# Performance work log

Measured on AMD Instinct MI355X. Metric: run time of the kernel, lower is better.

The kernel has to match this reference:

```python
import jax, jax.numpy as jnp
import numpy as np

B, N, NS, C, H = 2, 2048, 2048, 512, 8
HD = C // H
SCALE = HD ** -0.5
NEG = -10000.0


def setup_inputs() -> dict:
    key = jax.random.key(0)
    ks = jax.random.split(key, 9)
    q = jax.random.normal(ks[0], (B, N, C), dtype=jnp.float32)
    k = jax.random.normal(ks[1], (B, NS, C), dtype=jnp.float32)
    v = jax.random.normal(ks[2], (B, NS, C), dtype=jnp.float32)
    # 1.0 marks invalid support positions (gets -10000 added)
    supp_valid_mask = (jax.random.uniform(ks[3], (B, NS)) < 0.2).astype(jnp.float32)
    # binary fg/bg support mask used for cycle consistency
    supp_mask = jax.random.randint(ks[4], (B, NS), 0, 2, dtype=jnp.int32)
    w = 0.02
    Wq = jax.random.normal(ks[5], (C, C), dtype=jnp.float32) * w
    Wk = jax.random.normal(ks[6], (C, C), dtype=jnp.float32) * w
    Wv = jax.random.normal(ks[7], (C, C), dtype=jnp.float32) * w
    Wproj = jax.random.normal(ks[8], (C, C), dtype=jnp.float32) * w
    return {"q": q, "k": k, "v": v, "supp_valid_mask": supp_valid_mask,
            "supp_mask": supp_mask, "Wq": Wq, "Wk": Wk, "Wv": Wv, "Wproj": Wproj}


def reference(q, k, v, supp_valid_mask, supp_mask, Wq, Wk, Wv, Wproj):
    b, n, c = q.shape
    ns = k.shape[1]
    # linear projections (torch Linear: x @ W^T), split heads -> [B,H,N,HD]
    qh = (q @ Wq.T).reshape(b, n, H, HD).transpose(0, 2, 1, 3)
    kh = (k @ Wk.T).reshape(b, ns, H, HD).transpose(0, 2, 1, 3)
    vh = (v @ Wv.T).reshape(b, ns, H, HD).transpose(0, 2, 1, 3)
    attn = jnp.einsum('bhnd,bhmd->bhnm', qh, kh) * SCALE  # [B,H,N,NS]

    # cycle-consistency association (vectorized over heads)
    k2q = jnp.argmax(attn, axis=2)                    # [B,H,NS] idx into N
    q2k = jnp.argmax(attn, axis=3)                    # [B,H,N]  idx into NS
    re_map_idx = jnp.take_along_axis(q2k, k2q, axis=2)  # [B,H,NS]
    sm = jnp.broadcast_to(supp_mask[:, None, :], (b, H, ns))
    re_map_mask = jnp.take_along_axis(sm, re_map_idx, axis=2)
    asso = sm == re_map_mask                          # [B,H,NS] bool

    # mark cycle-inconsistent positions invalid (eval: ass_drop is identity)
    valid = jnp.broadcast_to(supp_valid_mask[:, None, :], (b, H, ns))
    valid = jnp.where(asso, valid, 1.0)

    attn = attn + (valid * NEG)[:, :, None, :]
    attn = jax.nn.softmax(attn, axis=-1)
    x = jnp.einsum('bhnm,bhmd->bhnd', attn, vh)       # [B,H,N,HD]
    x = x.transpose(0, 2, 1, 3).reshape(b, n, c)
    return x @ Wproj.T
```

## Files before the change

kernel.cpp:

```cpp
#include <hip/hip_runtime.h>
#include <hip/hip_bf16.h>
#include <stdint.h>

#define H_ 8
#define NS_ 2048
#define C_ 512
#define HD_ 64
#define SCALE_ 0.125f
#define NEG_ -10000.0f
#define LOG2E_ 1.4426950408889634f
#define MFIX_ 4.0f

typedef _Float16 f16x8_t __attribute__((ext_vector_type(8)));
typedef _Float16 f16x4_t __attribute__((ext_vector_type(4)));
typedef __fp16 h16x2_t __attribute__((ext_vector_type(2)));
typedef float f32x4_t __attribute__((ext_vector_type(4)));

#define MFMAH(a, b, c) __builtin_amdgcn_mfma_f32_16x16x32_f16(a, b, c, 0, 0, 0)

__device__ inline f16x8_t load_h8(const _Float16* p) {
    return *reinterpret_cast<const f16x8_t*>(p);
}

__device__ inline void gload_lds16(const void* g, void* l) {
    __builtin_amdgcn_global_load_lds(
        (const __attribute__((address_space(1))) unsigned int*)g,
        (__attribute__((address_space(3))) unsigned int*)l, 16, 0, 0);
}

__device__ inline unsigned orderF(float v) {
    unsigned u = __float_as_uint(v);
    return (u & 0x80000000u) ? ~u : (u | 0x80000000u);
}
__device__ inline unsigned long long packVR(float v, int idx) {
    return ((unsigned long long)orderF(v) << 32) | (unsigned)(~idx);
}
__device__ inline unsigned long long max64(unsigned long long a, unsigned long long b) {
    return a > b ? a : b;
}
__device__ inline unsigned long long shflx64(unsigned long long x, int m) {
    unsigned lo = (unsigned)x, hi = (unsigned)(x >> 32);
    lo = __shfl_xor(lo, m, 64);
    hi = __shfl_xor(hi, m, 64);
    return ((unsigned long long)hi << 32) | lo;
}

__global__ __launch_bounds__(256) void wsplit4(
        const float* __restrict__ w0, const float* __restrict__ w1,
        const float* __restrict__ w2, const float* __restrict__ w3,
        _Float16* __restrict__ hi, _Float16* __restrict__ lo)
{
    const int i = blockIdx.x * 256 + threadIdx.x;
    const int y = blockIdx.y;
    const float* src = (y == 0) ? w0 : (y == 1) ? w1 : (y == 2) ? w2 : w3;
    const float4 v = reinterpret_cast<const float4*>(src)[i];
    f16x4_t hv, lv;
    hv[0] = (_Float16)v.x; hv[1] = (_Float16)v.y;
    hv[2] = (_Float16)v.z; hv[3] = (_Float16)v.w;
    lv[0] = (_Float16)(v.x - (float)hv[0]);
    lv[1] = (_Float16)(v.y - (float)hv[1]);
    lv[2] = (_Float16)(v.z - (float)hv[2]);
    lv[3] = (_Float16)(v.w - (float)hv[3]);
    const size_t o = ((size_t)y << 16) + i;
    reinterpret_cast<f16x4_t*>(hi)[o] = hv;
    reinterpret_cast<f16x4_t*>(lo)[o] = lv;
}

__global__ __launch_bounds__(256) void proj_gemm(
        const float* __restrict__ qin, const float* __restrict__ kin,
        const float* __restrict__ vin,
        const _Float16* __restrict__ wHall, const _Float16* __restrict__ wLall,
        _Float16* __restrict__ qhi, _Float16* __restrict__ qlo,
        _Float16* __restrict__ khi, _Float16* __restrict__ klo,
        _Float16* __restrict__ vT)
{
    __shared__ __attribute__((aligned(16))) _Float16 Wsh[2][2][4096];
    const int zz = blockIdx.z;
    const float* A32 = (zz == 0) ? qin : (zz == 1) ? kin : vin;
    const _Float16* Wh = wHall + ((size_t)zz << 18);
    const _Float16* Wl = wLall + ((size_t)zz << 18);
    const int t = threadIdx.x, w = t >> 6, lane = t & 63;
    const int m16 = lane & 15, quad = lane >> 4;
    const int bm = blockIdx.x << 7, bn = blockIdx.y << 6;
    const int r0 = bm + (w << 5) + m16, r1 = r0 + 16;
    const int krow = lane >> 3, kblk = (lane & 7) ^ (krow & 7);
    const int e = m16 & 7;
    const int s00 = (quad ^ e) << 3, s01 = ((4 + quad) ^ e) << 3;
    const f32x4_t z = {0.f, 0.f, 0.f, 0.f};
    f32x4_t acc[2][4];
    #pragma unroll
    for (int rs = 0; rs < 2; rs++)
        #pragma unroll
        for (int tl = 0; tl < 4; tl++) acc[rs][tl] = z;

    auto stageW = [&](int buf, int kc) {
        #pragma unroll
        for (int ci = 0; ci < 4; ci++) {
            const int pp = (w << 2) + ci;
            const int s = pp >> 3, pj = pp & 7;
            const _Float16* src = (s ? Wl : Wh)
                + (size_t)(bn + (pj << 3) + krow) * C_ + kc + (kblk << 3);
            gload_lds16(src, &Wsh[buf][s][pj << 9]);
        }
    };
    auto loadA = [&](int kc, f16x8_t* d) {
        #pragma unroll
        for (int rs = 0; rs < 2; rs++) {
            const float* pr = A32 + (size_t)(rs ? r1 : r0) * C_ + kc + (quad << 3);
            #pragma unroll
            for (int seg = 0; seg < 2; seg++) {
                f16x8_t hv, lv;
                #pragma unroll
                for (int i = 0; i < 8; i++) {
                    const float x = pr[seg * 32 + i];
                    const _Float16 hh = (_Float16)x;
                    hv[i] = hh;
                    lv[i] = (_Float16)(x - (float)hh);
                }
                d[rs * 4 + seg] = hv;
                d[rs * 4 + seg + 2] = lv;
            }
        }
    };

    f16x8_t cA[8], nA[8];
    stageW(0, 0);
    loadA(0, cA);
    for (int ch = 0; ch < 8; ch++) {
        __syncthreads();
        if (ch + 1 < 8) {
            stageW((ch + 1) & 1, (ch + 1) << 6);
            loadA((ch + 1) << 6, nA);
        }
        const _Float16* W0 = Wsh[ch & 1][0];
        const _Float16* W1 = Wsh[ch & 1][1];
        #pragma unroll
        for (int tl = 0; tl < 4; tl++) {
            const int j64 = ((tl << 4) + m16) << 6;
            const f16x8_t bh0 = load_h8(&W0[j64 + s00]);
            const f16x8_t bh1 = load_h8(&W0[j64 + s01]);
            const f16x8_t bl0 = load_h8(&W1[j64 + s00]);
            const f16x8_t bl1 = load_h8(&W1[j64 + s01]);
            f32x4_t c0 = acc[0][tl];
            c0 = MFMAH(cA[0], bh0, c0); c0 = MFMAH(cA[1], bh1, c0);
            c0 = MFMAH(cA[2], bh0, c0); c0 = MFMAH(cA[3], bh1, c0);
            c0 = MFMAH(cA[0], bl0, c0); c0 = MFMAH(cA[1], bl1, c0);
            acc[0][tl] = c0;
            f32x4_t c1 = acc[1][tl];
            c1 = MFMAH(cA[4], bh0, c1); c1 = MFMAH(cA[5], bh1, c1);
            c1 = MFMAH(cA[6], bh0, c1); c1 = MFMAH(cA[7], bh1, c1);
            c1 = MFMAH(cA[4], bl0, c1); c1 = MFMAH(cA[5], bl1, c1);
            acc[1][tl] = c1;
        }
        #pragma unroll
        for (int i = 0; i < 8; i++) cA[i] = nA[i];
    }
    const int by = blockIdx.y;
    _Float16* o1 = (zz == 0) ? qhi : khi;
    _Float16* o2 = (zz == 0) ? qlo : klo;
    #pragma unroll
    for (int rs = 0; rs < 2; rs++) {
        #pragma unroll
        for (int tl = 0; tl < 4; tl++) {
            #pragma unroll
            for (int r = 0; r < 4; r++) {
                const int gr = bm + (w << 5) + (rs << 4) + (quad << 2) + r;
                const float val = acc[rs][tl][r];
                const int b = gr >> 11, n = gr & 2047;
                const int d = (tl << 4) + m16;
                const int bh = (b << 3) + by;
                if (zz == 2) {
                    const int kp = (((n >> 2) & 3) << 3) | (((n >> 4) & 1) << 2) | (n & 3);
                    vT[(((size_t)((bh << 6) + (n >> 5)) << 6) + d) * 32 + kp] = (_Float16)val;
                } else {
                    const size_t idx = ((((size_t)bh << 11) + n) << 6) + d;
                    const _Float16 hh = (_Float16)val;
                    o1[idx] = hh;
                    o2[idx] = (_Float16)(val - (float)hh);
                }
            }
        }
    }
}

__global__ __launch_bounds__(256) void argmax_mfma(
        const _Float16* __restrict__ qhi, const _Float16* __restrict__ qlo,
        const _Float16* __restrict__ khi, const _Float16* __restrict__ klo,
        unsigned long long* __restrict__ rowP, unsigned long long* __restrict__ colP)
{
    __shared__ __attribute__((aligned(16))) _Float16 Ksh[2][4096];
    __shared__ unsigned long long colbest[512];
    const int bx = blockIdx.x;
    const int bh = ((bx & 7) << 1) | (bx >> 9);
    const int mid = (bx >> 3) & 63;
    const int rt = mid & 15;
    const int ks = mid >> 4;
    const int t = threadIdx.x, w = t >> 6, lane = t & 63;
    const int m16 = lane & 15, quad = lane >> 4;
    const int wrow = (rt << 7) + (w << 5);
    const size_t qoff0 = ((((size_t)bh << 11) + wrow + m16) << 6) + (quad << 3);
    const size_t qoff1 = qoff0 + 1024;
    const f16x8_t a00h = load_h8(qhi + qoff0), a01h = load_h8(qhi + qoff0 + 32);
    const f16x8_t a00l = load_h8(qlo + qoff0), a01l = load_h8(qlo + qoff0 + 32);
    const f16x8_t a10h = load_h8(qhi + qoff1), a11h = load_h8(qhi + qoff1 + 32);
    const f16x8_t a10l = load_h8(qlo + qoff1), a11l = load_h8(qlo + qoff1 + 32);
    for (int c = t; c < 512; c += 256) colbest[c] = 0;
    const int krow = lane >> 3, kblk = (lane & 7) ^ (krow & 7);
    const int e = m16 & 7;
    const int s00 = (quad ^ e) << 3, s01 = ((4 + quad) ^ e) << 3;
    const size_t kbase = (((size_t)bh << 11) + (ks << 9)) << 6;
    float bv0[4] = {-3.4e38f, -3.4e38f, -3.4e38f, -3.4e38f};
    float bv1[4] = {-3.4e38f, -3.4e38f, -3.4e38f, -3.4e38f};
    int bc0[4] = {0, 0, 0, 0}, bc1[4] = {0, 0, 0, 0};
    const f32x4_t z = {0.f, 0.f, 0.f, 0.f};

    auto stage = [&](int cidx) {
        const size_t ce = kbase + ((size_t)cidx << 12);
        #pragma unroll
        for (int ci = 0; ci < 4; ci++) {
            const int pp = (w << 2) + ci;
            const int s = pp >> 3, pj = pp & 7;
            const _Float16* src = (s ? klo : khi) + ce + (((pj << 3) + krow) << 6) + (kblk << 3);
            gload_lds16(src, &Ksh[s][pj << 9]);
        }
    };

    for (int ch = 0; ch < 8; ch++) {
        __syncthreads();
        stage(ch);
        asm volatile("s_waitcnt vmcnt(0)" ::: "memory");
        __syncthreads();
        const _Float16* K0 = Ksh[0];
        const _Float16* K1 = Ksh[1];
        const int kc0 = (ks << 9) + (ch << 6);
        #pragma unroll
        for (int tl = 0; tl < 4; tl++) {
            const int j64 = ((tl << 4) + m16) << 6;
            const f16x8_t bh0 = load_h8(&K0[j64 + s00]);
            const f16x8_t bh1 = load_h8(&K0[j64 + s01]);
            const f16x8_t bl0 = load_h8(&K1[j64 + s00]);
            const f16x8_t bl1 = load_h8(&K1[j64 + s01]);
            f32x4_t c0 = MFMAH(a00h, bh0, z);
            c0 = MFMAH(a01h, bh1, c0);
            c0 = MFMAH(a00l, bh0, c0); c0 = MFMAH(a01l, bh1, c0);
            c0 = MFMAH(a00h, bl0, c0); c0 = MFMAH(a01h, bl1, c0);
            f32x4_t c1 = MFMAH(a10h, bh0, z);
            c1 = MFMAH(a11h, bh1, c1);
            c1 = MFMAH(a10l, bh0, c1); c1 = MFMAH(a11l, bh1, c1);
            c1 = MFMAH(a10h, bl0, c1); c1 = MFMAH(a11h, bl1, c1);
            const int gc = kc0 + (tl << 4) + m16;
            #pragma unroll
            for (int r = 0; r < 4; r++) {
                if (c0[r] > bv0[r]) { bv0[r] = c0[r]; bc0[r] = gc; }
                if (c1[r] > bv1[r]) { bv1[r] = c1[r]; bc1[r] = gc; }
            }
            float v = c0[0]; int ri = (quad << 2);
            if (c0[1] > v) { v = c0[1]; ri = (quad << 2) + 1; }
            if (c0[2] > v) { v = c0[2]; ri = (quad << 2) + 2; }
            if (c0[3] > v) { v = c0[3]; ri = (quad << 2) + 3; }
            if (c1[0] > v) { v = c1[0]; ri = 16 + (quad << 2); }
            if (c1[1] > v) { v = c1[1]; ri = 16 + (quad << 2) + 1; }
            if (c1[2] > v) { v = c1[2]; ri = 16 + (quad << 2) + 2; }
            if (c1[3] > v) { v = c1[3]; ri = 16 + (quad << 2) + 3; }
            unsigned long long pk = packVR(v, wrow + ri);
            pk = max64(pk, shflx64(pk, 16));
            pk = max64(pk, shflx64(pk, 32));
            if (quad == 0) atomicMax(&colbest[(ch << 6) + (tl << 4) + m16], pk);
        }
    }
    #pragma unroll
    for (int r = 0; r < 4; r++) {
        unsigned long long p0 = packVR(bv0[r], bc0[r]);
        p0 = max64(p0, shflx64(p0, 1)); p0 = max64(p0, shflx64(p0, 2));
        p0 = max64(p0, shflx64(p0, 4)); p0 = max64(p0, shflx64(p0, 8));
        if (m16 == 0)
            atomicMax(rowP + ((size_t)bh << 11) + wrow + (quad << 2) + r, p0);
        unsigned long long p1 = packVR(bv1[r], bc1[r]);
        p1 = max64(p1, shflx64(p1, 1)); p1 = max64(p1, shflx64(p1, 2));
        p1 = max64(p1, shflx64(p1, 4)); p1 = max64(p1, shflx64(p1, 8));
        if (m16 == 0)
            atomicMax(rowP + ((size_t)bh << 11) + wrow + 16 + (quad << 2) + r, p1);
    }
    __syncthreads();
    for (int c = t; c < 512; c += 256)
        atomicMax(colP + ((size_t)bh << 11) + (ks << 9) + c, colbest[c]);
}

__global__ __launch_bounds__(256, 4) void attn_pv(
        const _Float16* __restrict__ qh, const _Float16* __restrict__ kh,
        const _Float16* __restrict__ vT,
        const unsigned long long* __restrict__ q2kP,
        const unsigned long long* __restrict__ k2qP,
        const int* __restrict__ supp_mask,
        const float* __restrict__ supp_valid,
        float* __restrict__ xp, float* __restrict__ lp)
{
    __shared__ __attribute__((aligned(16))) _Float16 Ksh[2][4096];
    __shared__ __attribute__((aligned(16))) _Float16 Vsh[2][4096];
    __shared__ __attribute__((aligned(16))) float vnL[512];
    const int bx = blockIdx.x;
    const int bh = ((bx & 7) << 1) | (bx >> 9);
    const int mid = (bx >> 3) & 63;
    const int rt = mid & 15, ks = mid >> 4;
    const int t = threadIdx.x, w = t >> 6, lane = t & 63;
    const int m16 = lane & 15, quad = lane >> 4;
    const int rowbase = (rt << 7) + (w << 5);
    const size_t qoff = ((((size_t)bh << 11) + rowbase + m16) << 6) + (quad << 3);
    const f16x8_t a0 = load_h8(qh + qoff), a1 = load_h8(qh + qoff + 32);
    const f16x8_t a2 = load_h8(qh + qoff + 1024), a3 = load_h8(qh + qoff + 1056);
    {
        const int b = bh >> 3;
        for (int c = t; c < 512; c += 256) {
            const int j = (ks << 9) + c;
            const unsigned k2q = 0xFFFFFFFFu
                - (unsigned)(k2qP[(bh << 11) + j] & 0xFFFFFFFFull);
            const unsigned rm = 0xFFFFFFFFu
                - (unsigned)(q2kP[(bh << 11) + (int)k2q] & 0xFFFFFFFFull);
            const int asso = supp_mask[(b << 11) + j] == supp_mask[(b << 11) + (int)rm];
            const float valid = asso ? supp_valid[(b << 11) + j] : 1.0f;
            vnL[c] = fmaf(valid, NEG_ * LOG2E_, -MFIX_);
        }
    }
    const float KS = SCALE_ * LOG2E_;
    const int krow = lane >> 3, kblk = (lane & 7) ^ ((lane >> 3) & 7);
    const int vrow = lane >> 2, vblk = (lane & 3) ^ ((lane >> 3) & 3);
    const int e = m16 & 7;
    const int s00 = (quad ^ e) << 3, s01 = ((4 + quad) ^ e) << 3;
    const int vsw = (m16 >> 1) & 3;
    f16x8_t ones;
    #pragma unroll
    for (int i = 0; i < 8; i++) ones[i] = (_Float16)1.0f;
    const f32x4_t z = {0.f, 0.f, 0.f, 0.f};
    f32x4_t xacc0[4], xacc1[4];
    #pragma unroll
    for (int nt = 0; nt < 4; nt++) { xacc0[nt] = z; xacc1[nt] = z; }
    f32x4_t lacc0 = z, lacc1 = z;

    const size_t kbel = ((size_t)bh << 11) * HD_;
    const bool isK = (w < 2);
    const _Float16* src;
    _Float16* dstBase;
    if (isK) {
        src = kh + kbel + ((size_t)ks << 15) + (w << 11) + (krow << 6) + (kblk << 3);
        dstBase = &Ksh[0][w << 11];
    } else {
        src = vT + (((size_t)(bh << 6) + (ks << 4)) << 11)
                 + ((w - 2) << 11) + (vrow << 5) + (vblk << 3);
        dstBase = &Vsh[0][(w - 2) << 11];
    }
    auto stage = [&](int bufidx) {
        _Float16* d = dstBase + (bufidx << 12);
        gload_lds16(src, d);
        gload_lds16(src + 512, d + 512);
        gload_lds16(src + 1024, d + 1024);
        gload_lds16(src + 1536, d + 1536);
        src += 4096;
    };

    __syncthreads();
    stage(0);
    for (int ch = 0; ch < 8; ch++) {
        asm volatile("s_waitcnt vmcnt(0)" ::: "memory");
        __builtin_amdgcn_sched_barrier(0);
        __builtin_amdgcn_s_barrier();
        __builtin_amdgcn_sched_barrier(0);
        if (ch + 1 < 8) stage((ch + 1) & 1);
        #pragma unroll
        for (int hf = 0; hf < 2; hf++) {
            const _Float16* K = &Ksh[ch & 1][hf << 11];
            const _Float16* V = &Vsh[ch & 1][hf << 11];
            const f16x8_t b00 = load_h8(&K[(m16 << 6) + s00]);
            const f16x8_t b01 = load_h8(&K[(m16 << 6) + s01]);
            const f16x8_t b10 = load_h8(&K[((16 + m16) << 6) + s00]);
            const f16x8_t b11 = load_h8(&K[((16 + m16) << 6) + s01]);
            f32x4_t c0 = MFMAH(b00, a0, z); c0 = MFMAH(b01, a1, c0);
            f32x4_t c1 = MFMAH(b10, a0, z); c1 = MFMAH(b11, a1, c1);
            f32x4_t c2 = MFMAH(b00, a2, z); c2 = MFMAH(b01, a3, c2);
            f32x4_t c3 = MFMAH(b10, a2, z); c3 = MFMAH(b11, a3, c3);
            const int vb = (ch << 6) + (hf << 5);
            const f32x4_t vn0 = *reinterpret_cast<const f32x4_t*>(&vnL[vb + (quad << 2)]);
            const f32x4_t vn1 = *reinterpret_cast<const f32x4_t*>(&vnL[vb + 16 + (quad << 2)]);
            union { h16x2_t h2[4]; f16x8_t v8; } pk0, pk1;
            pk0.h2[0] = __builtin_amdgcn_cvt_pkrtz(
                __builtin_amdgcn_exp2f(fmaf(c0[0], KS, vn0[0])),
                __builtin_amdgcn_exp2f(fmaf(c0[1], KS, vn0[1])));
            pk0.h2[1] = __builtin_amdgcn_cvt_pkrtz(
                __builtin_amdgcn_exp2f(fmaf(c0[2], KS, vn0[2])),
                __builtin_amdgcn_exp2f(fmaf(c0[3], KS, vn0[3])));
            pk0.h2[2] = __builtin_amdgcn_cvt_pkrtz(
                __builtin_amdgcn_exp2f(fmaf(c1[0], KS, vn1[0])),
                __builtin_amdgcn_exp2f(fmaf(c1[1], KS, vn1[1])));
            pk0.h2[3] = __builtin_amdgcn_cvt_pkrtz(
                __builtin_amdgcn_exp2f(fmaf(c1[2], KS, vn1[2])),
                __builtin_amdgcn_exp2f(fmaf(c1[3], KS, vn1[3])));
            pk1.h2[0] = __builtin_amdgcn_cvt_pkrtz(
                __builtin_amdgcn_exp2f(fmaf(c2[0], KS, vn0[0])),
                __builtin_amdgcn_exp2f(fmaf(c2[1], KS, vn0[1])));
            pk1.h2[1] = __builtin_amdgcn_cvt_pkrtz(
                __builtin_amdgcn_exp2f(fmaf(c2[2], KS, vn0[2])),
                __builtin_amdgcn_exp2f(fmaf(c2[3], KS, vn0[3])));
            pk1.h2[2] = __builtin_amdgcn_cvt_pkrtz(
                __builtin_amdgcn_exp2f(fmaf(c3[0], KS, vn1[0])),
                __builtin_amdgcn_exp2f(fmaf(c3[1], KS, vn1[1])));
            pk1.h2[3] = __builtin_amdgcn_cvt_pkrtz(
                __builtin_amdgcn_exp2f(fmaf(c3[2], KS, vn1[2])),
                __builtin_amdgcn_exp2f(fmaf(c3[3], KS, vn1[3])));
            const f16x8_t pa0 = pk0.v8, pa1 = pk1.v8;
            lacc0 = MFMAH(pa0, ones, lacc0);
            lacc1 = MFMAH(pa1, ones, lacc1);
            #pragma unroll
            for (int nt = 0; nt < 4; nt++) {
                const f16x8_t vb2 = load_h8(&V[((nt * 16 + m16) << 5) + ((quad ^ vsw) << 3)]);
                xacc0[nt] = MFMAH(pa0, vb2, xacc0[nt]);
                xacc1[nt] = MFMAH(pa1, vb2, xacc1[nt]);
            }
        }
    }
    const int b = bh >> 3, h = bh & 7;
    if (m16 == 0) {
        #pragma unroll
        for (int r = 0; r < 4; r++) {
            lp[((size_t)ks << 15) + (bh << 11) + rowbase + (quad << 2) + r] = lacc0[r];
            lp[((size_t)ks << 15) + (bh << 11) + rowbase + 16 + (quad << 2) + r] = lacc1[r];
        }
    }
    const size_t xbase = ((size_t)ks << 21);
    #pragma unroll
    for (int r = 0; r < 4; r++) {
        const int row0 = rowbase + (quad << 2) + r;
        const int row1 = row0 + 16;
        #pragma unroll
        for (int nt = 0; nt < 4; nt++) {
            xp[xbase + (((size_t)(b << 11) + row0) << 9) + (h << 6) + (nt << 4) + m16] = xacc0[nt][r];
            xp[xbase + (((size_t)(b << 11) + row1) << 9) + (h << 6) + (nt << 4) + m16] = xacc1[nt][r];
        }
    }
}

__global__ __launch_bounds__(256) void combine4(
        const float* __restrict__ xp, const float* __restrict__ lp,
        _Float16* __restrict__ Ahi, _Float16* __restrict__ Alo)
{
    const int gid = blockIdx.x * 256 + threadIdx.x;
    const int r = gid >> 6, c8 = gid & 63;
    const int b = r >> 11, n = r & 2047, h = c8 >> 3;
    const size_t li = ((size_t)((b << 3) + h) << 11) + n;
    const float linv = 1.0f / (lp[li] + lp[32768 + li] + lp[65536 + li] + lp[98304 + li]);
    const size_t o = (size_t)gid << 3;
    const float4* x0 = reinterpret_cast<const float4*>(xp + o);
    const float4* x1 = reinterpret_cast<const float4*>(xp + 2097152 + o);
    const float4* x2 = reinterpret_cast<const float4*>(xp + 4194304 + o);
    const float4* x3 = reinterpret_cast<const float4*>(xp + 6291456 + o);
    f16x8_t hv, lv;
    #pragma unroll
    for (int s = 0; s < 2; s++) {
        const float4 p0 = x0[s], p1 = x1[s], p2 = x2[s], p3 = x3[s];
        float vv[4];
        vv[0] = (p0.x + p1.x + p2.x + p3.x) * linv;
        vv[1] = (p0.y + p1.y + p2.y + p3.y) * linv;
        vv[2] = (p0.z + p1.z + p2.z + p3.z) * linv;
        vv[3] = (p0.w + p1.w + p2.w + p3.w) * linv;
        #pragma unroll
        for (int i = 0; i < 4; i++) {
            const _Float16 hh = (_Float16)vv[i];
            hv[s * 4 + i] = hh;
            lv[s * 4 + i] = (_Float16)(vv[i] - (float)hh);
        }
    }
    *reinterpret_cast<f16x8_t*>(Ahi + o) = hv;
    *reinterpret_cast<f16x8_t*>(Alo + o) = lv;
}

__global__ __launch_bounds__(256) void out_gemm(
        const _Float16* __restrict__ Ahi, const _Float16* __restrict__ Alo,
        const _Float16* __restrict__ Wh, const _Float16* __restrict__ Wl,
        float* __restrict__ outF)
{
    __shared__ __attribute__((aligned(16))) _Float16 Wsh[2][2][4096];
    const int t = threadIdx.x, w = t >> 6, lane = t & 63;
    const int m16 = lane & 15, quad = lane >> 4;
    const int bm = blockIdx.x << 7, bn = blockIdx.y << 6;
    const int r0 = bm + (w << 5) + m16, r1 = r0 + 16;
    const int krow = lane >> 3, kblk = (lane & 7) ^ (krow & 7);
    const int e = m16 & 7;
    const int s00 = (quad ^ e) << 3, s01 = ((4 + quad) ^ e) << 3;
    const f32x4_t z = {0.f, 0.f, 0.f, 0.f};
    f32x4_t acc[2][4];
    #pragma unroll
    for (int rs = 0; rs < 2; rs++)
        #pragma unroll
        for (int tl = 0; tl < 4; tl++) acc[rs][tl] = z;

    auto stageW = [&](int buf, int kc) {
        #pragma unroll
        for (int ci = 0; ci < 4; ci++) {
            const int pp = (w << 2) + ci;
            const int s = pp >> 3, pj = pp & 7;
            const _Float16* src = (s ? Wl : Wh)
                + (size_t)(bn + (pj << 3) + krow) * C_ + kc + (kblk << 3);
            gload_lds16(src, &Wsh[buf][s][pj << 9]);
        }
    };
    auto loadA = [&](int ch, f16x8_t* d) {
        const int kc = ch << 6;
        #pragma unroll
        for (int rs = 0; rs < 2; rs++) {
            const size_t base = ((size_t)(rs ? r1 : r0) << 9) + kc + (quad << 3);
            d[rs * 4 + 0] = load_h8(Ahi + base);
            d[rs * 4 + 1] = load_h8(Ahi + base + 32);
            d[rs * 4 + 2] = load_h8(Alo + base);
            d[rs * 4 + 3] = load_h8(Alo + base + 32);
        }
    };

    f16x8_t cA[8], nA[8];
    stageW(0, 0);
    loadA(0, cA);
    for (int ch = 0; ch < 8; ch++) {
        __syncthreads();
        if (ch + 1 < 8) {
            stageW((ch + 1) & 1, (ch + 1) << 6);
            loadA(ch + 1, nA);
        }
        const _Float16* W0 = Wsh[ch & 1][0];
        const _Float16* W1 = Wsh[ch & 1][1];
        #pragma unroll
        for (int tl = 0; tl < 4; tl++) {
            const int j64 = ((tl << 4) + m16) << 6;
            const f16x8_t bh0 = load_h8(&W0[j64 + s00]);
            const f16x8_t bh1 = load_h8(&W0[j64 + s01]);
            const f16x8_t bl0 = load_h8(&W1[j64 + s00]);
            const f16x8_t bl1 = load_h8(&W1[j64 + s01]);
            f32x4_t c0 = acc[0][tl];
            c0 = MFMAH(cA[0], bh0, c0); c0 = MFMAH(cA[1], bh1, c0);
            c0 = MFMAH(cA[2], bh0, c0); c0 = MFMAH(cA[3], bh1, c0);
            c0 = MFMAH(cA[0], bl0, c0); c0 = MFMAH(cA[1], bl1, c0);
            acc[0][tl] = c0;
            f32x4_t c1 = acc[1][tl];
            c1 = MFMAH(cA[4], bh0, c1); c1 = MFMAH(cA[5], bh1, c1);
            c1 = MFMAH(cA[6], bh0, c1); c1 = MFMAH(cA[7], bh1, c1);
            c1 = MFMAH(cA[4], bl0, c1); c1 = MFMAH(cA[5], bl1, c1);
            acc[1][tl] = c1;
        }
        #pragma unroll
        for (int i = 0; i < 8; i++) cA[i] = nA[i];
    }
    #pragma unroll
    for (int rs = 0; rs < 2; rs++) {
        #pragma unroll
        for (int tl = 0; tl < 4; tl++) {
            #pragma unroll
            for (int r = 0; r < 4; r++) {
                const int gr = bm + (w << 5) + (rs << 4) + (quad << 2) + r;
                const int gj = bn + (tl << 4) + m16;
                outF[(size_t)gr * C_ + gj] = acc[rs][tl][r];
            }
        }
    }
}

extern "C" void kernel_launch(void* const* d_in, const int* in_sizes, int n_in,
                              void* d_out, int out_size, void* d_ws, size_t ws_size,
                              hipStream_t stream) {
    const float* q  = (const float*)d_in[0];
    const float* k  = (const float*)d_in[1];
    const float* v  = (const float*)d_in[2];
    const float* supp_valid = (const float*)d_in[3];
    const int*   supp_mask  = (const int*)d_in[4];
    const float* Wq = (const float*)d_in[5];
    const float* Wk = (const float*)d_in[6];
    const float* Wv = (const float*)d_in[7];
    const float* Wp = (const float*)d_in[8];
    float* out = (float*)d_out;

    char* p = (char*)d_ws;
    _Float16* qhi = (_Float16*)p;      p += 4194304;
    _Float16* qlo = (_Float16*)p;      p += 4194304;
    _Float16* khi = (_Float16*)p;      p += 4194304;
    _Float16* klo = (_Float16*)p;      p += 4194304;
    _Float16* vT  = (_Float16*)p;      p += 4194304;
    float* xp     = (float*)p;         p += 33554432;
    _Float16* wH  = (_Float16*)p;      p += 2097152;
    _Float16* wL  = (_Float16*)p;      p += 2097152;
    _Float16* Ahi = (_Float16*)p;      p += 4194304;
    _Float16* Alo = (_Float16*)p;      p += 4194304;
    unsigned long long* q2kP = (unsigned long long*)p; p += 262144;
    unsigned long long* k2qP = (unsigned long long*)p; p += 262144;
    float* lp = (float*)p;             p += 524288;

    (void)hipMemsetAsync(q2kP, 0, 524288, stream);

    dim3 bG(256);
    wsplit4<<<dim3(256, 4), bG, 0, stream>>>(Wq, Wk, Wv, Wp, wH, wL);
    proj_gemm<<<dim3(32, 8, 3), bG, 0, stream>>>(q, k, v, wH, wL,
                                                 qhi, qlo, khi, klo, vT);

    argmax_mfma<<<1024, bG, 0, stream>>>(qhi, qlo, khi, klo, q2kP, k2qP);

    attn_pv<<<1024, bG, 0, stream>>>(qhi, khi, vT, q2kP, k2qP,
                                     supp_mask, supp_valid, xp, lp);

    combine4<<<1024, bG, 0, stream>>>(xp, lp, Ahi, Alo);

    out_gemm<<<dim3(32, 8), bG, 0, stream>>>(Ahi, Alo,
                                             wH + 3 * 262144, wL + 3 * 262144, out);
}
```

Baseline: 203.8 us.

## Double rows per warp in attn_pv to reuse K/V tiles across more queries

Each warp in attn_pv now handles 64 query rows (four 16-row slabs) instead of 32, so each block covers 256 rows and the grid shrinks from 1024 to 512 blocks. Every K/V tile staged into shared memory and every V fragment read from LDS is reused across twice as many MFMAs, and the vnL mask setup and K/V global traffic per query row are halved. In exchange each thread holds twice the accumulators and Q fragments, so launch bounds drop to 2 blocks per SM, lowering occupancy, and fewer blocks may leave the GPU underfilled.

```diff
diff --git a/kernel.cpp b/kernel.cpp
--- a/kernel.cpp
+++ b/kernel.cpp
@@ -286,7 +286,7 @@
         atomicMax(colP + ((size_t)bh << 11) + (ks << 9) + c, colbest[c]);
 }
 
-__global__ __launch_bounds__(256, 4) void attn_pv(
+__global__ __launch_bounds__(256, 2) void attn_pv(
         const _Float16* __restrict__ qh, const _Float16* __restrict__ kh,
         const _Float16* __restrict__ vT,
         const unsigned long long* __restrict__ q2kP,
@@ -299,15 +299,19 @@
     __shared__ __attribute__((aligned(16))) _Float16 Vsh[2][4096];
     __shared__ __attribute__((aligned(16))) float vnL[512];
     const int bx = blockIdx.x;
-    const int bh = ((bx & 7) << 1) | (bx >> 9);
-    const int mid = (bx >> 3) & 63;
-    const int rt = mid & 15, ks = mid >> 4;
+    const int bh = ((bx & 7) << 1) | (bx >> 8);
+    const int mid = (bx >> 3) & 31;
+    const int rt = mid & 7, ks = mid >> 3;
     const int t = threadIdx.x, w = t >> 6, lane = t & 63;
     const int m16 = lane & 15, quad = lane >> 4;
-    const int rowbase = (rt << 7) + (w << 5);
+    const int rowbase = (rt << 8) + (w << 6);
     const size_t qoff = ((((size_t)bh << 11) + rowbase + m16) << 6) + (quad << 3);
-    const f16x8_t a0 = load_h8(qh + qoff), a1 = load_h8(qh + qoff + 32);
-    const f16x8_t a2 = load_h8(qh + qoff + 1024), a3 = load_h8(qh + qoff + 1056);
+    f16x8_t aF[8];
+    #pragma unroll
+    for (int rs = 0; rs < 4; rs++) {
+        aF[2 * rs]     = load_h8(qh + qoff + rs * 1024);
+        aF[2 * rs + 1] = load_h8(qh + qoff + rs * 1024 + 32);
+    }
     {
         const int b = bh >> 3;
         for (int c = t; c < 512; c += 256) {
@@ -331,10 +335,14 @@
     #pragma unroll
     for (int i = 0; i < 8; i++) ones[i] = (_Float16)1.0f;
     const f32x4_t z = {0.f, 0.f, 0.f, 0.f};
-    f32x4_t xacc0[4], xacc1[4];
-    #pragma unroll
-    for (int nt = 0; nt < 4; nt++) { xacc0[nt] = z; xacc1[nt] = z; }
-    f32x4_t lacc0 = z, lacc1 = z;
+    f32x4_t xacc[4][4];
+    #pragma unroll
+    for (int rs = 0; rs < 4; rs++)
+        #pragma unroll
+        for (int nt = 0; nt < 4; nt++) xacc[rs][nt] = z;
+    f32x4_t lacc[4];
+    #pragma unroll
+    for (int rs = 0; rs < 4; rs++) lacc[rs] = z;
 
     const size_t kbel = ((size_t)bh << 11) * HD_;
     const bool isK = (w < 2);
@@ -373,66 +381,60 @@
             const f16x8_t b01 = load_h8(&K[(m16 << 6) + s01]);
             const f16x8_t b10 = load_h8(&K[((16 + m16) << 6) + s00]);
             const f16x8_t b11 = load_h8(&K[((16 + m16) << 6) + s01]);
-            f32x4_t c0 = MFMAH(b00, a0, z); c0 = MFMAH(b01, a1, c0);
-            f32x4_t c1 = MFMAH(b10, a0, z); c1 = MFMAH(b11, a1, c1);
-            f32x4_t c2 = MFMAH(b00, a2, z); c2 = MFMAH(b01, a3, c2);
-            f32x4_t c3 = MFMAH(b10, a2, z); c3 = MFMAH(b11, a3, c3);
             const int vb = (ch << 6) + (hf << 5);
             const f32x4_t vn0 = *reinterpret_cast<const f32x4_t*>(&vnL[vb + (quad << 2)]);
             const f32x4_t vn1 = *reinterpret_cast<const f32x4_t*>(&vnL[vb + 16 + (quad << 2)]);
-            union { h16x2_t h2[4]; f16x8_t v8; } pk0, pk1;
-            pk0.h2[0] = __builtin_amdgcn_cvt_pkrtz(
-                __builtin_amdgcn_exp2f(fmaf(c0[0], KS, vn0[0])),
-                __builtin_amdgcn_exp2f(fmaf(c0[1], KS, vn0[1])));
-            pk0.h2[1] = __builtin_amdgcn_cvt_pkrtz(
-                __builtin_amdgcn_exp2f(fmaf(c0[2], KS, vn0[2])),
-                __builtin_amdgcn_exp2f(fmaf(c0[3], KS, vn0[3])));
-            pk0.h2[2] = __builtin_amdgcn_cvt_pkrtz(
-                __builtin_amdgcn_exp2f(fmaf(c1[0], KS, vn1[0])),
-                __builtin_amdgcn_exp2f(fmaf(c1[1], KS, vn1[1])));
-            pk0.h2[3] = __builtin_amdgcn_cvt_pkrtz(
-                __builtin_amdgcn_exp2f(fmaf(c1[2], KS, vn1[2])),
-                __builtin_amdgcn_exp2f(fmaf(c1[3], KS, vn1[3])));
-            pk1.h2[0] = __builtin_amdgcn_cvt_pkrtz(
-                __builtin_amdgcn_exp2f(fmaf(c2[0], KS, vn0[0])),
-                __builtin_amdgcn_exp2f(fmaf(c2[1], KS, vn0[1])));
-            pk1.h2[1] = __builtin_amdgcn_cvt_pkrtz(
-                __builtin_amdgcn_exp2f(fmaf(c2[2], KS, vn0[2])),
-                __builtin_amdgcn_exp2f(fmaf(c2[3], KS, vn0[3])));
-            pk1.h2[2] = __builtin_amdgcn_cvt_pkrtz(
-                __builtin_amdgcn_exp2f(fmaf(c3[0], KS, vn1[0])),
-                __builtin_amdgcn_exp2f(fmaf(c3[1], KS, vn1[1])));
-            pk1.h2[3] = __builtin_amdgcn_cvt_pkrtz(
-                __builtin_amdgcn_exp2f(fmaf(c3[2], KS, vn1[2])),
-                __builtin_amdgcn_exp2f(fmaf(c3[3], KS, vn1[3])));
-            const f16x8_t pa0 = pk0.v8, pa1 = pk1.v8;
-            lacc0 = MFMAH(pa0, ones, lacc0);
-            lacc1 = MFMAH(pa1, ones, lacc1);
+            f16x8_t pa[4];
+            #pragma unroll
+            for (int rs = 0; rs < 4; rs++) {
+                f32x4_t cA = MFMAH(b00, aF[2 * rs], z);
+                cA = MFMAH(b01, aF[2 * rs + 1], cA);
+                f32x4_t cB = MFMAH(b10, aF[2 * rs], z);
+                cB = MFMAH(b11, aF[2 * rs + 1], cB);
+                union { h16x2_t h2[4]; f16x8_t v8; } pk;
+                pk.h2[0] = __builtin_amdgcn_cvt_pkrtz(
+                    __builtin_amdgcn_exp2f(fmaf(cA[0], KS, vn0[0])),
+                    __builtin_amdgcn_exp2f(fmaf(cA[1], KS, vn0[1])));
+                pk.h2[1] = __builtin_amdgcn_cvt_pkrtz(
+                    __builtin_amdgcn_exp2f(fmaf(cA[2], KS, vn0[2])),
+                    __builtin_amdgcn_exp2f(fmaf(cA[3], KS, vn0[3])));
+                pk.h2[2] = __builtin_amdgcn_cvt_pkrtz(
+                    __builtin_amdgcn_exp2f(fmaf(cB[0], KS, vn1[0])),
+                    __builtin_amdgcn_exp2f(fmaf(cB[1], KS, vn1[1])));
+                pk.h2[3] = __builtin_amdgcn_cvt_pkrtz(
+                    __builtin_amdgcn_exp2f(fmaf(cB[2], KS, vn1[2])),
+                    __builtin_amdgcn_exp2f(fmaf(cB[3], KS, vn1[3])));
+                pa[rs] = pk.v8;
+                lacc[rs] = MFMAH(pa[rs], ones, lacc[rs]);
+            }
             #pragma unroll
             for (int nt = 0; nt < 4; nt++) {
                 const f16x8_t vb2 = load_h8(&V[((nt * 16 + m16) << 5) + ((quad ^ vsw) << 3)]);
-                xacc0[nt] = MFMAH(pa0, vb2, xacc0[nt]);
-                xacc1[nt] = MFMAH(pa1, vb2, xacc1[nt]);
+                #pragma unroll
+                for (int rs = 0; rs < 4; rs++)
+                    xacc[rs][nt] = MFMAH(pa[rs], vb2, xacc[rs][nt]);
             }
         }
     }
     const int b = bh >> 3, h = bh & 7;
     if (m16 == 0) {
         #pragma unroll
+        for (int rs = 0; rs < 4; rs++)
+            #pragma unroll
+            for (int r = 0; r < 4; r++)
+                lp[((size_t)ks << 15) + (bh << 11) + rowbase + (rs << 4) + (quad << 2) + r]
+                    = lacc[rs][r];
+    }
+    const size_t xbase = ((size_t)ks << 21);
+    #pragma unroll
+    for (int rs = 0; rs < 4; rs++) {
+        #pragma unroll
         for (int r = 0; r < 4; r++) {
-            lp[((size_t)ks << 15) + (bh << 11) + rowbase + (quad << 2) + r] = lacc0[r];
-            lp[((size_t)ks << 15) + (bh << 11) + rowbase + 16 + (quad << 2) + r] = lacc1[r];
-        }
-    }
-    const size_t xbase = ((size_t)ks << 21);
-    #pragma unroll
-    for (int r = 0; r < 4; r++) {
-        const int row0 = rowbase + (quad << 2) + r;
-        const int row1 = row0 + 16;
-        #pragma unroll
-        for (int nt = 0; nt < 4; nt++) {
-            xp[xbase + (((size_t)(b << 11) + row0) << 9) + (h << 6) + (nt << 4) + m16] = xacc0[nt][r];
-            xp[xbase + (((size_t)(b << 11) + row1) << 9) + (h << 6) + (nt << 4) + m16] = xacc1[nt][r];
+            const int row = rowbase + (rs << 4) + (quad << 2) + r;
+            #pragma unroll
+            for (int nt = 0; nt < 4; nt++)
+                xp[xbase + (((size_t)(b << 11) + row) << 9) + (h << 6) + (nt << 4) + m16]
+                    = xacc[rs][nt][r];
         }
     }
 }
@@ -597,8 +599,8 @@
 
     argmax_mfma<<<1024, bG, 0, stream>>>(qhi, qlo, khi, klo, q2kP, k2qP);
 
-    attn_pv<<<1024, bG, 0, stream>>>(qhi, khi, vT, q2kP, k2qP,
-                                     supp_mask, supp_valid, xp, lp);
+    attn_pv<<<512, bG, 0, stream>>>(qhi, khi, vT, q2kP, k2qP,
+                                    supp_mask, supp_valid, xp, lp);
 
     combine4<<<1024, bG, 0, stream>>>(xp, lp, Ahi, Alo);
 
```

Measured after the change: 207.8 us. Within noise of the previous version (+1.9%).
